# Optimization experiments

Hardware: AMD Instinct MI355X
Metric: run time of the kernel (lower is better)

The kernel has to match this reference:

```python
import jax, jax.numpy as jnp
import numpy as np


def setup_inputs() -> dict:
    key = jax.random.key(0)
    k1, k2, k3 = jax.random.split(key, 3)
    B, N, M = 8, 4096, 4096
    recon = jax.random.normal(k1, (B, M, 3), dtype=jnp.float32)
    src_points = jax.random.normal(k2, (B, N, 3), dtype=jnp.float32)
    transform = jax.random.normal(k3, (B, 4, 4), dtype=jnp.float32)
    return {"recon": recon, "src_points": src_points, "transform": transform}


def _apply_transform(points, transform):
    # points: [B,N,3], transform: [B,4,4] -> p @ R^T + t
    R = transform[:, :3, :3]   # [B,3,3]
    t = transform[:, :3, 3]    # [B,3]
    return jnp.einsum('bnd,bkd->bnk', points, R) + t[:, None, :]


def reference(recon, src_points, transform):
    gts = _apply_transform(src_points, transform)  # [B,N,3]
    preds = recon                                   # [B,M,3]
    # pairwise squared distances P[b,i,j] = |gts_i|^2 + |preds_j|^2 - 2 gts_i . preds_j
    xx = jnp.sum(gts * gts, axis=-1)                # [B,N]
    yy = jnp.sum(preds * preds, axis=-1)            # [B,M]
    zz = jnp.einsum('bnd,bmd->bnm', gts, preds)     # [B,N,M]
    P = xx[:, :, None] + yy[:, None, :] - 2.0 * zz  # [B,N,M]
    loss_1 = jnp.sum(jnp.min(P, axis=1))            # min over gts for each pred
    loss_2 = jnp.sum(jnp.min(P, axis=2))            # min over preds for each gt
    return loss_1 + loss_2
```

## Files before the change

kernel.cpp:

```cpp
#include <hip/hip_runtime.h>
#include <math.h>

#define TPB      256
#define KA       8
#define QPB      (TPB * KA)
#define C_CHUNKS 32
#define MAX_CPTS 128

__global__ __launch_bounds__(TPB) void prep_kernel(
    const float* __restrict__ recon,
    const float* __restrict__ src,
    const float* __restrict__ T,
    float4* __restrict__ preds,
    float4* __restrict__ gts,
    float* __restrict__ out, int out_n,
    int B, int N, int M)
{
    int idx = blockIdx.x * TPB + threadIdx.x;
    if (idx < out_n) out[idx] = 0.0f;
    int totG = B * N;
    int totP = B * M;
    if (idx < totG) {
        int b = idx / N;
        const float* Tb = T + b * 16;
        float x = src[3*idx + 0], y = src[3*idx + 1], z = src[3*idx + 2];
        float gx = fmaf(Tb[0], x, fmaf(Tb[1], y, fmaf(Tb[2],  z, Tb[3])));
        float gy = fmaf(Tb[4], x, fmaf(Tb[5], y, fmaf(Tb[6],  z, Tb[7])));
        float gz = fmaf(Tb[8], x, fmaf(Tb[9], y, fmaf(Tb[10], z, Tb[11])));
        gts[idx] = make_float4(gx, gy, gz, fmaf(gx, gx, fmaf(gy, gy, gz * gz)));
    } else if (idx - totG < totP) {
        int k = idx - totG;
        float x = recon[3*k + 0], y = recon[3*k + 1], z = recon[3*k + 2];
        preds[k] = make_float4(x, y, z, fmaf(x, x, fmaf(y, y, z * z)));
    }
}

__global__ __launch_bounds__(TPB) void chamfer_kernel(
    const float4* __restrict__ gts,
    const float4* __restrict__ preds,
    float* __restrict__ partial,
    int B, int N, int M, int GQ)
{
    __shared__ float4 sB[MAX_CPTS];

    const int dir = blockIdx.z;
    const int b   = blockIdx.y;
    const int c   = blockIdx.x % C_CHUNKS;
    const int qt  = blockIdx.x / C_CHUNKS;

    const int NA  = (dir == 0) ? N : M;
    const int NB_ = (dir == 0) ? M : N;
    if (qt * QPB >= NA) return;

    const float4* __restrict__ Aset = (dir == 0) ? (gts   + (size_t)b * N) : (preds + (size_t)b * M);
    const float4* __restrict__ Bset = (dir == 0) ? (preds + (size_t)b * M) : (gts   + (size_t)b * N);
    const int gq_base = ((dir == 0) ? 0 : B * N) + b * NA;

    const int cpts = (NB_ + C_CHUNKS - 1) / C_CHUNKS;
    const int j0   = c * cpts;
    const int jn   = (j0 + cpts <= NB_) ? cpts : (NB_ - j0);
    for (int t = threadIdx.x; t < jn; t += TPB) sB[t] = Bset[j0 + t];
    __syncthreads();

    int   qi[KA];
    float a2x[KA], a2y[KA], a2z[KA], aw[KA];
    #pragma unroll
    for (int k = 0; k < KA; ++k) {
        qi[k] = qt * QPB + k * TPB + (int)threadIdx.x;
        float4 a = (qi[k] < NA) ? Aset[qi[k]] : make_float4(0.f, 0.f, 0.f, 0.f);
        a2x[k] = -2.0f * a.x; a2y[k] = -2.0f * a.y; a2z[k] = -2.0f * a.z; aw[k] = a.w;
    }

    float mA[KA], mB[KA];
    #pragma unroll
    for (int k = 0; k < KA; ++k) { mA[k] = INFINITY; mB[k] = INFINITY; }

    int j = 0;
    const int jn4 = jn & ~3;
    for (; j < jn4; j += 4) {
        float4 b0 = sB[j+0], b1 = sB[j+1], b2 = sB[j+2], b3 = sB[j+3];
        #pragma unroll
        for (int k = 0; k < KA; ++k) {
            float d0 = fmaf(a2x[k], b0.x, fmaf(a2y[k], b0.y, fmaf(a2z[k], b0.z, b0.w)));
            float d1 = fmaf(a2x[k], b1.x, fmaf(a2y[k], b1.y, fmaf(a2z[k], b1.z, b1.w)));
            float d2 = fmaf(a2x[k], b2.x, fmaf(a2y[k], b2.y, fmaf(a2z[k], b2.z, b2.w)));
            float d3 = fmaf(a2x[k], b3.x, fmaf(a2y[k], b3.y, fmaf(a2z[k], b3.z, b3.w)));
            mA[k] = fminf(fminf(mA[k], d0), d1);
            mB[k] = fminf(fminf(mB[k], d2), d3);
        }
    }
    for (; j < jn; ++j) {
        float4 bj = sB[j];
        #pragma unroll
        for (int k = 0; k < KA; ++k) {
            float d = fmaf(a2x[k], bj.x, fmaf(a2y[k], bj.y, fmaf(a2z[k], bj.z, bj.w)));
            mA[k] = fminf(mA[k], d);
        }
    }

    #pragma unroll
    for (int k = 0; k < KA; ++k) {
        if (qi[k] < NA)
            partial[(size_t)c * GQ + gq_base + qi[k]] = aw[k] + fminf(mA[k], mB[k]);
    }
}

__global__ __launch_bounds__(TPB) void reduce_kernel(
    const float* __restrict__ partial, float* __restrict__ out, int GQ)
{
    int q = blockIdx.x * TPB + threadIdx.x;
    float m = 0.0f;
    if (q < GQ) {
        m = partial[q];
        #pragma unroll
        for (int c = 1; c < C_CHUNKS; ++c)
            m = fminf(m, partial[(size_t)c * GQ + q]);
    }
    #pragma unroll
    for (int off = 32; off > 0; off >>= 1) m += __shfl_down(m, off);
    __shared__ float red[TPB / 64];
    if ((threadIdx.x & 63) == 0) red[threadIdx.x >> 6] = m;
    __syncthreads();
    if (threadIdx.x == 0) {
        float s = 0.0f;
        #pragma unroll
        for (int w = 0; w < TPB / 64; ++w) s += red[w];
        atomicAdd(out, s);
    }
}

extern "C" void kernel_launch(void* const* d_in, const int* in_sizes, int n_in,
                              void* d_out, int out_size, void* d_ws, size_t ws_size,
                              hipStream_t stream)
{
    const float* recon = (const float*)d_in[0];
    const float* src   = (const float*)d_in[1];
    const float* T     = (const float*)d_in[2];

    const int B = in_sizes[2] / 16;
    const int M = in_sizes[0] / (B * 3);
    const int N = in_sizes[1] / (B * 3);
    const int GQ = B * (N + M);

    float4* preds   = (float4*)d_ws;
    float4* gts     = preds + (size_t)B * M;
    float*  partial = (float*)(gts + (size_t)B * N);
    float*  out     = (float*)d_out;

    prep_kernel<<<dim3((GQ + TPB - 1) / TPB), dim3(TPB), 0, stream>>>(
        recon, src, T, preds, gts, out, out_size, B, N, M);

    const int NAmax = (N > M) ? N : M;
    const int QT    = (NAmax + QPB - 1) / QPB;
    dim3 grid(QT * C_CHUNKS, B, 2);
    chamfer_kernel<<<grid, dim3(TPB), 0, stream>>>(gts, preds, partial, B, N, M, GQ);

    reduce_kernel<<<dim3((GQ + TPB - 1) / TPB), dim3(TPB), 0, stream>>>(partial, out, GQ);
}
```

Measured before the change: 89.68 us.

## Use chunked SoA layout and packed FP32 FMA in chamfer inner loop

Prep now writes points in a chunked structure-of-arrays layout (128-point tiles with x, y, z and norm planes), so each block loads its tile with one float4 copy. The inner loop uses inline v_pk_fma_f32 to evaluate two candidate points per instruction, which roughly halves VALU FMA count. It also adds a launch-bounds occupancy hint. Bounds checks and tail handling are removed, so the code assumes N and M are multiples of 128 and 2048.

```diff
diff --git a/kernel.cpp b/kernel.cpp
--- a/kernel.cpp
+++ b/kernel.cpp
@@ -1,18 +1,21 @@
 #include <hip/hip_runtime.h>
 #include <math.h>
 
-#define TPB      256
-#define KA       8
-#define QPB      (TPB * KA)
-#define C_CHUNKS 32
-#define MAX_CPTS 128
+#define TPB       256
+#define KA        8
+#define QPB       (TPB * KA)
+#define C_CHUNKS  32
+#define CPTS      128
+#define CHUNK_F   (CPTS * 4)
+
+typedef float v2f __attribute__((ext_vector_type(2)));
 
 __global__ __launch_bounds__(TPB) void prep_kernel(
     const float* __restrict__ recon,
     const float* __restrict__ src,
     const float* __restrict__ T,
-    float4* __restrict__ preds,
-    float4* __restrict__ gts,
+    float* __restrict__ preds_soa,
+    float* __restrict__ gts_soa,
     float* __restrict__ out, int out_n,
     int B, int N, int M)
 {
@@ -21,27 +24,36 @@
     int totG = B * N;
     int totP = B * M;
     if (idx < totG) {
-        int b = idx / N;
+        int b = idx / N, n = idx - b * N;
         const float* Tb = T + b * 16;
         float x = src[3*idx + 0], y = src[3*idx + 1], z = src[3*idx + 2];
         float gx = fmaf(Tb[0], x, fmaf(Tb[1], y, fmaf(Tb[2],  z, Tb[3])));
         float gy = fmaf(Tb[4], x, fmaf(Tb[5], y, fmaf(Tb[6],  z, Tb[7])));
         float gz = fmaf(Tb[8], x, fmaf(Tb[9], y, fmaf(Tb[10], z, Tb[11])));
-        gts[idx] = make_float4(gx, gy, gz, fmaf(gx, gx, fmaf(gy, gy, gz * gz)));
+        size_t base = ((size_t)b * (N / CPTS) + (n >> 7)) * CHUNK_F + (n & 127);
+        gts_soa[base      ] = gx;
+        gts_soa[base + 128] = gy;
+        gts_soa[base + 256] = gz;
+        gts_soa[base + 384] = fmaf(gx, gx, fmaf(gy, gy, gz * gz));
     } else if (idx - totG < totP) {
         int k = idx - totG;
+        int b = k / M, m = k - b * M;
         float x = recon[3*k + 0], y = recon[3*k + 1], z = recon[3*k + 2];
-        preds[k] = make_float4(x, y, z, fmaf(x, x, fmaf(y, y, z * z)));
+        size_t base = ((size_t)b * (M / CPTS) + (m >> 7)) * CHUNK_F + (m & 127);
+        preds_soa[base      ] = x;
+        preds_soa[base + 128] = y;
+        preds_soa[base + 256] = z;
+        preds_soa[base + 384] = fmaf(x, x, fmaf(y, y, z * z));
     }
 }
 
-__global__ __launch_bounds__(TPB) void chamfer_kernel(
-    const float4* __restrict__ gts,
-    const float4* __restrict__ preds,
+__global__ __launch_bounds__(TPB, 4) void chamfer_kernel(
+    const float* __restrict__ gts_soa,
+    const float* __restrict__ preds_soa,
     float* __restrict__ partial,
     int B, int N, int M, int GQ)
 {
-    __shared__ float4 sB[MAX_CPTS];
+    __shared__ __align__(16) float sL[CHUNK_F];
 
     const int dir = blockIdx.z;
     const int b   = blockIdx.y;
@@ -52,56 +64,58 @@
     const int NB_ = (dir == 0) ? M : N;
     if (qt * QPB >= NA) return;
 
-    const float4* __restrict__ Aset = (dir == 0) ? (gts   + (size_t)b * N) : (preds + (size_t)b * M);
-    const float4* __restrict__ Bset = (dir == 0) ? (preds + (size_t)b * M) : (gts   + (size_t)b * N);
+    const float* __restrict__ Asoa = (dir == 0) ? gts_soa : preds_soa;
+    const float* __restrict__ Bsoa = (dir == 0) ? preds_soa : gts_soa;
     const int gq_base = ((dir == 0) ? 0 : B * N) + b * NA;
 
-    const int cpts = (NB_ + C_CHUNKS - 1) / C_CHUNKS;
-    const int j0   = c * cpts;
-    const int jn   = (j0 + cpts <= NB_) ? cpts : (NB_ - j0);
-    for (int t = threadIdx.x; t < jn; t += TPB) sB[t] = Bset[j0 + t];
+    {
+        const float4* gsrc = (const float4*)(Bsoa + ((size_t)b * (NB_ / CPTS) + c) * CHUNK_F);
+        if (threadIdx.x < CPTS) ((float4*)sL)[threadIdx.x] = gsrc[threadIdx.x];
+    }
     __syncthreads();
 
-    int   qi[KA];
-    float a2x[KA], a2y[KA], a2z[KA], aw[KA];
+    float aw[KA], mA[KA], mB[KA];
+    v2f A2X[KA], A2Y[KA], A2Z[KA];
+    int qi0 = qt * QPB + (int)threadIdx.x;
     #pragma unroll
     for (int k = 0; k < KA; ++k) {
-        qi[k] = qt * QPB + k * TPB + (int)threadIdx.x;
-        float4 a = (qi[k] < NA) ? Aset[qi[k]] : make_float4(0.f, 0.f, 0.f, 0.f);
-        a2x[k] = -2.0f * a.x; a2y[k] = -2.0f * a.y; a2z[k] = -2.0f * a.z; aw[k] = a.w;
+        int q = qi0 + k * TPB;
+        const float* ab = Asoa + ((size_t)b * (NA / CPTS) + (q >> 7)) * CHUNK_F + (q & 127);
+        float ax = ab[0], ay = ab[128], az = ab[256];
+        aw[k] = ab[384];
+        float tx = -2.0f * ax, ty = -2.0f * ay, tz = -2.0f * az;
+        A2X[k].x = tx; A2X[k].y = tx;
+        A2Y[k].x = ty; A2Y[k].y = ty;
+        A2Z[k].x = tz; A2Z[k].y = tz;
+        mA[k] = INFINITY; mB[k] = INFINITY;
     }
 
-    float mA[KA], mB[KA];
-    #pragma unroll
-    for (int k = 0; k < KA; ++k) { mA[k] = INFINITY; mB[k] = INFINITY; }
+    const v2f* sX = (const v2f*)(sL +   0);
+    const v2f* sY = (const v2f*)(sL + 128);
+    const v2f* sZ = (const v2f*)(sL + 256);
+    const v2f* sW = (const v2f*)(sL + 384);
 
-    int j = 0;
-    const int jn4 = jn & ~3;
-    for (; j < jn4; j += 4) {
-        float4 b0 = sB[j+0], b1 = sB[j+1], b2 = sB[j+2], b3 = sB[j+3];
+    for (int jj = 0; jj < CPTS / 2; jj += 2) {
+        v2f x0 = sX[jj],   y0 = sY[jj],   z0 = sZ[jj],   w0 = sW[jj];
+        v2f x1 = sX[jj+1], y1 = sY[jj+1], z1 = sZ[jj+1], w1 = sW[jj+1];
         #pragma unroll
         for (int k = 0; k < KA; ++k) {
-            float d0 = fmaf(a2x[k], b0.x, fmaf(a2y[k], b0.y, fmaf(a2z[k], b0.z, b0.w)));
-            float d1 = fmaf(a2x[k], b1.x, fmaf(a2y[k], b1.y, fmaf(a2z[k], b1.z, b1.w)));
-            float d2 = fmaf(a2x[k], b2.x, fmaf(a2y[k], b2.y, fmaf(a2z[k], b2.z, b2.w)));
-            float d3 = fmaf(a2x[k], b3.x, fmaf(a2y[k], b3.y, fmaf(a2z[k], b3.z, b3.w)));
-            mA[k] = fminf(fminf(mA[k], d0), d1);
-            mB[k] = fminf(fminf(mB[k], d2), d3);
-        }
-    }
-    for (; j < jn; ++j) {
-        float4 bj = sB[j];
-        #pragma unroll
-        for (int k = 0; k < KA; ++k) {
-            float d = fmaf(a2x[k], bj.x, fmaf(a2y[k], bj.y, fmaf(a2z[k], bj.z, bj.w)));
-            mA[k] = fminf(mA[k], d);
+            v2f d0, d1;
+            asm("v_pk_fma_f32 %0, %1, %2, %3" : "=v"(d0) : "v"(A2Z[k]), "v"(z0), "v"(w0));
+            asm("v_pk_fma_f32 %0, %1, %2, %0" : "+v"(d0) : "v"(A2Y[k]), "v"(y0));
+            asm("v_pk_fma_f32 %0, %1, %2, %0" : "+v"(d0) : "v"(A2X[k]), "v"(x0));
+            asm("v_pk_fma_f32 %0, %1, %2, %3" : "=v"(d1) : "v"(A2Z[k]), "v"(z1), "v"(w1));
+            asm("v_pk_fma_f32 %0, %1, %2, %0" : "+v"(d1) : "v"(A2Y[k]), "v"(y1));
+            asm("v_pk_fma_f32 %0, %1, %2, %0" : "+v"(d1) : "v"(A2X[k]), "v"(x1));
+            mA[k] = fminf(fminf(mA[k], d0.x), d0.y);
+            mB[k] = fminf(fminf(mB[k], d1.x), d1.y);
         }
     }
 
     #pragma unroll
     for (int k = 0; k < KA; ++k) {
-        if (qi[k] < NA)
-            partial[(size_t)c * GQ + gq_base + qi[k]] = aw[k] + fminf(mA[k], mB[k]);
+        int q = qi0 + k * TPB;
+        partial[(size_t)c * GQ + gq_base + q] = aw[k] + fminf(mA[k], mB[k]);
     }
 }
 
@@ -142,18 +156,18 @@
     const int N = in_sizes[1] / (B * 3);
     const int GQ = B * (N + M);
 
-    float4* preds   = (float4*)d_ws;
-    float4* gts     = preds + (size_t)B * M;
-    float*  partial = (float*)(gts + (size_t)B * N);
-    float*  out     = (float*)d_out;
+    float* preds_soa = (float*)d_ws;
+    float* gts_soa   = preds_soa + (size_t)B * M * 4;
+    float* partial   = gts_soa + (size_t)B * N * 4;
+    float* out       = (float*)d_out;
 
     prep_kernel<<<dim3((GQ + TPB - 1) / TPB), dim3(TPB), 0, stream>>>(
-        recon, src, T, preds, gts, out, out_size, B, N, M);
+        recon, src, T, preds_soa, gts_soa, out, out_size, B, N, M);
 
     const int NAmax = (N > M) ? N : M;
     const int QT    = (NAmax + QPB - 1) / QPB;
     dim3 grid(QT * C_CHUNKS, B, 2);
-    chamfer_kernel<<<grid, dim3(TPB), 0, stream>>>(gts, preds, partial, B, N, M, GQ);
+    chamfer_kernel<<<grid, dim3(TPB), 0, stream>>>(gts_soa, preds_soa, partial, B, N, M, GQ);
 
     reduce_kernel<<<dim3((GQ + TPB - 1) / TPB), dim3(TPB), 0, stream>>>(partial, out, GQ);
 }
```

After: 87.94 us. Within noise of the previous version (-1.9%).
